# Performance work log

Hardware: AMD Instinct MI355X
Metric: run time of the kernel (lower is better)

Reference implementation:

```python
import jax, jax.numpy as jnp
import numpy as np

CPJ = 8
HID = 256
PARENTS = [-1,0,0,0,1,2,3,4,5,6,7,8,9,9,9,12,13,14,16,17,18,19]
SPARSE_IDX = list(range(54))

def _extend(nodes, cpj, parents=None):
    nodes = list(nodes)
    if parents is not None:
        while nodes[-1] != 0:
            nodes.append(parents[nodes[-1]])
    return [j * cpj + k for j in nodes for k in range(cpj)]

DQ_IN = _extend([0,3,6,9,12,13,14,15,16,17,18,19,20,21], CPJ, PARENTS)  # 21 nodes -> 168 ch
OUT1 = _extend([9], CPJ)          # 8 ch
OUT2 = _extend([6, 9, 12], CPJ)   # 24 ch
OUT3 = _extend([0, 3, 6], CPJ)    # 24 ch
IN_DIM = len(DQ_IN) + len(SPARSE_IDX)  # 222


def _mlp_params(key, out_dim):
    k = jax.random.split(key, 6)
    s = lambda fan_in: 1.0 / np.sqrt(fan_in)
    return (
        jax.random.uniform(k[0], (IN_DIM, HID), jnp.float32, -s(IN_DIM), s(IN_DIM)),
        jax.random.uniform(k[1], (HID,), jnp.float32, -s(IN_DIM), s(IN_DIM)),
        jax.random.uniform(k[2], (HID, HID), jnp.float32, -s(HID), s(HID)),
        jax.random.uniform(k[3], (HID,), jnp.float32, -s(HID), s(HID)),
        jax.random.uniform(k[4], (HID, out_dim), jnp.float32, -s(HID), s(HID)),
        jax.random.uniform(k[5], (out_dim,), jnp.float32, -s(HID), s(HID)),
    )


def setup_inputs() -> dict:
    key = jax.random.key(0)
    ks = jax.random.split(key, 5)
    B, T = 1024, 128
    inp = {
        'sparse_input': jax.random.normal(ks[0], (B, T, 54), jnp.float32),
        'decoder_output': jax.random.normal(ks[1], (B, T, 22 * CPJ), jnp.float32),
    }
    for i, (k, od) in enumerate(zip(ks[2:5], (len(OUT1), len(OUT2), len(OUT3))), start=1):
        p = _mlp_params(k, od)
        for j, name in enumerate(('w0', 'b0', 'w1', 'b1', 'w2', 'b2')):
            inp[f'{name}_{i}'] = p[j]
    return inp


def _mlp(x, w0, b0, w1, b1, w2, b2):
    h = jax.nn.leaky_relu(x @ w0 + b0, 0.01)
    h = jax.nn.leaky_relu(h @ w1 + b1, 0.01)
    return h @ w2 + b2


def reference(sparse_input, decoder_output,
              w0_1, b0_1, w1_1, b1_1, w2_1, b2_1,
              w0_2, b0_2, w1_2, b1_2, w2_2, b2_2,
              w0_3, b0_3, w1_3, b1_3, w2_3, b2_3):
    sp = sparse_input[:, :, jnp.array(SPARSE_IDX)]
    d = decoder_output
    # pass 1
    x = jnp.concatenate((d[:, :, jnp.array(DQ_IN)], sp), axis=2)
    res1 = _mlp(x, w0_1, b0_1, w1_1, b1_1, w2_1, b2_1)
    d = d.at[:, :, jnp.array(OUT1)].set(res1)
    # pass 2
    x = jnp.concatenate((d[:, :, jnp.array(DQ_IN)], sp), axis=2)
    res2 = _mlp(x, w0_2, b0_2, w1_2, b1_2, w2_2, b2_2)
    d = d.at[:, :, jnp.array(OUT2)].set(res2)
    # pass 3
    x = jnp.concatenate((d[:, :, jnp.array(DQ_IN)], sp), axis=2)
    res3 = _mlp(x, w0_3, b0_3, w1_3, b1_3, w2_3, b2_3)
    return res3
```

## Files before the change

### kernel.cpp

```cpp
#include <hip/hip_runtime.h>

typedef __bf16 bf16x8 __attribute__((ext_vector_type(8)));
typedef __bf16 bf16x4 __attribute__((ext_vector_type(4)));
typedef float  f32x16 __attribute__((ext_vector_type(16)));

#define DDEC  176
#define DSP   54
#define HID   256
#define RPW   32
#define WPB   8
#define BM    (RPW * WPB)
#define NTHR  (WPB * 64)
#define CSZ   8192
#define W1_OFF 65536
#define W2_OFF 131072
#define MLP_WS 139264

struct Biases { const float* b1[3]; const float* b2[3]; };

__global__ __launch_bounds__(256) void prep_weights(
    const float* __restrict__ w0a, const float* __restrict__ w1a, const float* __restrict__ w2a,
    const float* __restrict__ w0b, const float* __restrict__ w1b, const float* __restrict__ w2b,
    const float* __restrict__ w0c, const float* __restrict__ w1c, const float* __restrict__ w2c,
    const float* __restrict__ b0a, const float* __restrict__ b0b, const float* __restrict__ b0c,
    __bf16* __restrict__ ws)
{
  int idx = blockIdx.x * 256 + threadIdx.x;
  if (idx >= 3 * MLP_WS) return;
  int m = idx / MLP_WS;
  int r = idx - m * MLP_WS;
  const float* w0 = (m == 0) ? w0a : (m == 1) ? w0b : w0c;
  const float* w1 = (m == 0) ? w1a : (m == 1) ? w1b : w1c;
  const float* w2 = (m == 0) ? w2a : (m == 1) ? w2b : w2c;
  const float* b0 = (m == 0) ? b0a : (m == 1) ? b0b : b0c;
  float v;
  if (r < W1_OFF) {
    int n = r >> 8, k = r & 255;
    v = (k < 222) ? w0[k * HID + n] : (k == 222 ? b0[n] : 0.0f);
  } else if (r < W2_OFF) {
    int rr = r - W1_OFF;
    int n = rr >> 8, k = rr & 255;
    v = w1[k * HID + n];
  } else {
    int rr = r - W2_OFF;
    int n = rr >> 8, k = rr & 255;
    int od = (m == 0) ? 8 : 24;
    v = (n < od) ? w2[k * od + n] : 0.0f;
  }
  ws[idx] = (__bf16)v;
}

__device__ __forceinline__ float lrelu(float v) { return v > 0.f ? v : 0.01f * v; }

__device__ __forceinline__ void gload16(const void* g, void* l) {
  __builtin_amdgcn_global_load_lds(
      (const __attribute__((address_space(1))) void*)g,
      (__attribute__((address_space(3))) void*)l, 16, 0, 0);
}

__device__ __forceinline__ void stage(const __bf16* __restrict__ wsrc, __bf16* buf, int tid) {
  #pragma unroll
  for (int r = 0; r < 2; ++r) {
    const int a  = (r * NTHR + tid) * 16;
    const int lc = a >> 9;
    const int un = (a & 511) ^ ((lc & 31) << 4);
    gload16(wsrc + lc * 256 + (un >> 1), (char*)buf + r * (NTHR * 16) + (tid >> 6) * 1024);
  }
}

template<int NKK>
__device__ __forceinline__ void gemm1(const __bf16* buf, const bf16x8* bfr,
                                      f32x16& acc, int r32, int h) {
  const int sw = r32 << 4;
  const char* abase = (const char*)buf + (r32 << 9);
  #pragma unroll
  for (int kk = 0; kk < NKK; ++kk) {
    const int inner = ((kk << 5) + (h << 4)) ^ sw;
    bf16x8 a0 = *(const bf16x8*)(abase + inner);
    acc = __builtin_amdgcn_mfma_f32_32x32x16_bf16(a0, bfr[kk], acc, 0, 0, 0);
  }
}

__device__ __forceinline__ bf16x4 shfl32(bf16x4 x) {
  union { bf16x4 v; unsigned long long u; } t;
  t.v = x;
  t.u = __shfl_xor(t.u, 32, 64);
  return t.v;
}
__device__ __forceinline__ bf16x8 cat44(bf16x4 lo, bf16x4 hi) {
  return (bf16x8){lo[0], lo[1], lo[2], lo[3], hi[0], hi[1], hi[2], hi[3]};
}

struct Frag2 { bf16x8 f0, f1; };

template<bool BIAS, bool LR>
__device__ __forceinline__ Frag2 d2frags(const f32x16 acc, const float* bias, int h) {
  bf16x4 pk[4];
  #pragma unroll
  for (int t = 0; t < 4; ++t) {
    float bx = 0.f, by = 0.f, bz = 0.f, bw = 0.f;
    if (BIAS) {
      float4 bv = *(const float4*)(bias + 8 * t + 4 * h);
      bx = bv.x; by = bv.y; bz = bv.z; bw = bv.w;
    }
    float v0 = acc[4 * t] + bx, v1 = acc[4 * t + 1] + by;
    float v2 = acc[4 * t + 2] + bz, v3 = acc[4 * t + 3] + bw;
    if (LR) { v0 = lrelu(v0); v1 = lrelu(v1); v2 = lrelu(v2); v3 = lrelu(v3); }
    pk[t] = (bf16x4){(__bf16)v0, (__bf16)v1, (__bf16)v2, (__bf16)v3};
  }
  bf16x4 r1 = shfl32(h ? pk[0] : pk[1]);
  bf16x4 r2 = shfl32(h ? pk[2] : pk[3]);
  Frag2 out;
  out.f0 = h ? cat44(r1, pk[1]) : cat44(pk[0], r1);
  out.f1 = h ? cat44(r2, pk[3]) : cat44(pk[2], r2);
  return out;
}

__device__ __forceinline__ bf16x8 packf44(float4 a, float4 b) {
  return (bf16x8){(__bf16)a.x, (__bf16)a.y, (__bf16)a.z, (__bf16)a.w,
                  (__bf16)b.x, (__bf16)b.y, (__bf16)b.z, (__bf16)b.w};
}
__device__ __forceinline__ bf16x8 packf2222(float2 a, float2 b, float2 c, float2 d) {
  return (bf16x8){(__bf16)a.x, (__bf16)a.y, (__bf16)b.x, (__bf16)b.y,
                  (__bf16)c.x, (__bf16)c.y, (__bf16)d.x, (__bf16)d.y};
}

__global__ __launch_bounds__(NTHR, 2) void trunk_fused(
    const float* __restrict__ sparse, const float* __restrict__ dec,
    const __bf16* __restrict__ ws, float* __restrict__ out, Biases bp)
{
  __shared__ __align__(16) __bf16 lds[2 * CSZ];
  __bf16* const buf0 = lds;
  __bf16* const buf1 = lds + CSZ;

  const int tid  = threadIdx.x;
  const int lane = tid & 63;
  const int wid  = tid >> 6;
  const int r32  = lane & 31;
  const int h    = lane >> 5;
  const long grow = (long)blockIdx.x * BM + wid * RPW + r32;

  stage(ws, buf0, tid);

  bf16x8 xb[14];
  {
    constexpr int ND[21] = {0,3,6,9,12,13,14,15,16,17,18,19,20,21,19,17,14,9,6,3,0};
    const float* drow = dec + grow * DDEC;
    const float* srow = sparse + grow * DSP;
    #pragma unroll
    for (int kf = 0; kf < 14; ++kf) {
      if (kf <= 9) {
        const int off = (h ? ND[2 * kf + 1] : ND[2 * kf]) * 8;
        const float4* p = (const float4*)(drow + off);
        xb[kf] = packf44(p[0], p[1]);
      } else if (kf == 10) {
        if (h == 0) {
          const float4* p = (const float4*)(drow + ND[20] * 8);
          xb[kf] = packf44(p[0], p[1]);
        } else {
          const float2* q = (const float2*)(srow + 0);
          xb[kf] = packf2222(q[0], q[1], q[2], q[3]);
        }
      } else if (kf <= 12) {
        const float2* q = (const float2*)(srow + (2 * kf + h - 21) * 8);
        xb[kf] = packf2222(q[0], q[1], q[2], q[3]);
      } else {
        if (h == 0) {
          const float2* q = (const float2*)(srow + 40);
          xb[kf] = packf2222(q[0], q[1], q[2], q[3]);
        } else {
          const float2* q = (const float2*)(srow + 48);
          xb[kf] = packf2222(q[0], q[1], q[2], make_float2(1.0f, 0.0f));
        }
      }
    }
  }
  __syncthreads();
  int pb = 0;

  for (int m = 0; m < 3; ++m) {
    const __bf16* W0 = ws + m * MLP_WS;
    const __bf16* W1 = W0 + W1_OFF;
    const __bf16* W2 = W0 + W2_OFF;
    const float* b1 = bp.b1[m];
    const float* b2 = bp.b2[m];

    bf16x8 hb1[16];
    f32x16 a2 = {};

    #pragma unroll
    for (int c = 0; c < 8; ++c) {
      __bf16* cur = pb ? buf1 : buf0;
      __bf16* nxt = pb ? buf0 : buf1;
      stage(c < 7 ? W0 + (c + 1) * CSZ : W1, nxt, tid);
      f32x16 acc = {};
      gemm1<14>(cur, xb, acc, r32, h);
      Frag2 t = d2frags<false, true>(acc, nullptr, h);
      hb1[2 * c]     = t.f0;
      hb1[2 * c + 1] = t.f1;
      __syncthreads();
      pb ^= 1;
    }

    #pragma unroll
    for (int c = 0; c < 8; ++c) {
      __bf16* cur = pb ? buf1 : buf0;
      __bf16* nxt = pb ? buf0 : buf1;
      const __bf16* w2f = W2 + r32 * 256 + h * 8 + 32 * c;
      bf16x8 wa0 = *(const bf16x8*)(w2f + 0);
      bf16x8 wa1 = *(const bf16x8*)(w2f + 16);
      if (c < 7)      stage(W1 + (c + 1) * CSZ, nxt, tid);
      else if (m < 2) stage(ws + (m + 1) * MLP_WS, nxt, tid);
      f32x16 acc = {};
      gemm1<16>(cur, hb1, acc, r32, h);
      Frag2 t = d2frags<true, true>(acc, b1 + 32 * c, h);
      a2 = __builtin_amdgcn_mfma_f32_32x32x16_bf16(wa0, t.f0, a2, 0, 0, 0);
      a2 = __builtin_amdgcn_mfma_f32_32x32x16_bf16(wa1, t.f1, a2, 0, 0, 0);
      __syncthreads();
      pb ^= 1;
    }

    if (m == 2) {
      #pragma unroll
      for (int t = 0; t < 3; ++t) {
        const int c0 = 8 * t + 4 * h;
        float4 bv = *(const float4*)(b2 + c0);
        float4 o;
        o.x = a2[4 * t]     + bv.x;
        o.y = a2[4 * t + 1] + bv.y;
        o.z = a2[4 * t + 2] + bv.z;
        o.w = a2[4 * t + 3] + bv.w;
        *(float4*)(out + grow * 24 + c0) = o;
      }
    } else {
      bf16x4 pk[3];
      #pragma unroll
      for (int t = 0; t < 3; ++t) {
        const int c0 = 8 * t + 4 * h;
        float4 bv = *(const float4*)(b2 + c0);
        pk[t] = (bf16x4){(__bf16)(a2[4 * t] + bv.x),     (__bf16)(a2[4 * t + 1] + bv.y),
                         (__bf16)(a2[4 * t + 2] + bv.z), (__bf16)(a2[4 * t + 3] + bv.w)};
      }
      if (m == 0) {
        bf16x4 r = shfl32(pk[0]);
        if (h) { bf16x8 f = cat44(r, pk[0]); xb[1] = f; xb[8] = f; }
      } else {
        bf16x4 r1 = shfl32(h ? pk[0] : pk[1]);
        bf16x4 r2 = shfl32(pk[2]);
        if (h) {
          bf16x8 fJ9 = cat44(r1, pk[1]);  xb[1] = fJ9;  xb[8] = fJ9;
        } else {
          bf16x8 fJ6  = cat44(pk[0], r1); xb[1] = fJ6;  xb[9] = fJ6;
          bf16x8 fJ12 = cat44(pk[2], r2); xb[2] = fJ12;
        }
      }
    }
  }
}

extern "C" void kernel_launch(void* const* d_in, const int* in_sizes, int n_in,
                              void* d_out, int out_size, void* d_ws, size_t ws_size,
                              hipStream_t stream)
{
  const float* sparse = (const float*)d_in[0];
  const float* dec    = (const float*)d_in[1];
  Biases bp;
  const float* w0[3]; const float* w1[3]; const float* w2[3]; const float* b0[3];
  for (int m = 0; m < 3; ++m) {
    w0[m]    = (const float*)d_in[2 + m * 6 + 0];
    b0[m]    = (const float*)d_in[2 + m * 6 + 1];
    w1[m]    = (const float*)d_in[2 + m * 6 + 2];
    bp.b1[m] = (const float*)d_in[2 + m * 6 + 3];
    w2[m]    = (const float*)d_in[2 + m * 6 + 4];
    bp.b2[m] = (const float*)d_in[2 + m * 6 + 5];
  }
  __bf16* ws = (__bf16*)d_ws;
  const int nrows = in_sizes[0] / DSP;

  const int prep_total = 3 * MLP_WS;
  prep_weights<<<(prep_total + 255) / 256, 256, 0, stream>>>(
      w0[0], w1[0], w2[0], w0[1], w1[1], w2[1], w0[2], w1[2], w2[2],
      b0[0], b0[1], b0[2], ws);

  const int nblocks = nrows / BM;
  trunk_fused<<<nblocks, NTHR, 0, stream>>>(sparse, dec, ws, (float*)d_out, bp);
}
```

Baseline: 132.5 us.

## Deepen weight-staging pipeline to four LDS buffers with counted vmcnt waits

Replaces the double-buffered weight staging with a four-slot LDS ring that keeps three chunks in flight. A unified chunk index handles addressing across all three MLPs. Each iteration waits with an s_waitcnt vmcnt(4) plus barrier instead of a full __syncthreads, so outstanding prefetches are not drained. This aims to hide global-to-LDS latency, but it doubles LDS per block, which may hurt occupancy, and it relies on exact counting of outstanding memory ops for correctness.

```diff
diff --git a/kernel.cpp b/kernel.cpp
--- a/kernel.cpp
+++ b/kernel.cpp
@@ -68,6 +68,15 @@
   }
 }
 
+#define WAIT_BAR() asm volatile("s_waitcnt vmcnt(4)\n\ts_barrier" ::: "memory")
+
+__device__ __forceinline__ const __bf16* srcp(const __bf16* ws, int g) {
+  if (g > 47) g = 0;
+  const int m = g >> 4, c = g & 15;
+  const __bf16* base = ws + m * MLP_WS;
+  return (c < 8) ? (base + c * CSZ) : (base + W1_OFF + (c - 8) * CSZ);
+}
+
 template<int NKK>
 __device__ __forceinline__ void gemm1(const __bf16* buf, const bf16x8* bfr,
                                       f32x16& acc, int r32, int h) {
@@ -129,9 +138,7 @@
     const float* __restrict__ sparse, const float* __restrict__ dec,
     const __bf16* __restrict__ ws, float* __restrict__ out, Biases bp)
 {
-  __shared__ __align__(16) __bf16 lds[2 * CSZ];
-  __bf16* const buf0 = lds;
-  __bf16* const buf1 = lds + CSZ;
+  __shared__ __align__(16) __bf16 lds[4 * CSZ];
 
   const int tid  = threadIdx.x;
   const int lane = tid & 63;
@@ -140,7 +147,9 @@
   const int h    = lane >> 5;
   const long grow = (long)blockIdx.x * BM + wid * RPW + r32;
 
-  stage(ws, buf0, tid);
+  stage(srcp(ws, 0), lds + 0 * CSZ, tid);
+  stage(srcp(ws, 1), lds + 1 * CSZ, tid);
+  stage(srcp(ws, 2), lds + 2 * CSZ, tid);
 
   bf16x8 xb[14];
   {
@@ -176,12 +185,10 @@
     }
   }
   __syncthreads();
-  int pb = 0;
-
+
+  #pragma unroll
   for (int m = 0; m < 3; ++m) {
-    const __bf16* W0 = ws + m * MLP_WS;
-    const __bf16* W1 = W0 + W1_OFF;
-    const __bf16* W2 = W0 + W2_OFF;
+    const __bf16* W2 = ws + m * MLP_WS + W2_OFF;
     const float* b1 = bp.b1[m];
     const float* b2 = bp.b2[m];
 
@@ -190,34 +197,29 @@
 
     #pragma unroll
     for (int c = 0; c < 8; ++c) {
-      __bf16* cur = pb ? buf1 : buf0;
-      __bf16* nxt = pb ? buf0 : buf1;
-      stage(c < 7 ? W0 + (c + 1) * CSZ : W1, nxt, tid);
+      const int g = m * 16 + c;
+      WAIT_BAR();
+      stage(srcp(ws, g + 3), lds + ((g + 3) & 3) * CSZ, tid);
       f32x16 acc = {};
-      gemm1<14>(cur, xb, acc, r32, h);
+      gemm1<14>(lds + (g & 3) * CSZ, xb, acc, r32, h);
       Frag2 t = d2frags<false, true>(acc, nullptr, h);
       hb1[2 * c]     = t.f0;
       hb1[2 * c + 1] = t.f1;
-      __syncthreads();
-      pb ^= 1;
     }
 
     #pragma unroll
     for (int c = 0; c < 8; ++c) {
-      __bf16* cur = pb ? buf1 : buf0;
-      __bf16* nxt = pb ? buf0 : buf1;
+      const int g = m * 16 + 8 + c;
+      WAIT_BAR();
+      stage(srcp(ws, g + 3), lds + ((g + 3) & 3) * CSZ, tid);
       const __bf16* w2f = W2 + r32 * 256 + h * 8 + 32 * c;
       bf16x8 wa0 = *(const bf16x8*)(w2f + 0);
       bf16x8 wa1 = *(const bf16x8*)(w2f + 16);
-      if (c < 7)      stage(W1 + (c + 1) * CSZ, nxt, tid);
-      else if (m < 2) stage(ws + (m + 1) * MLP_WS, nxt, tid);
       f32x16 acc = {};
-      gemm1<16>(cur, hb1, acc, r32, h);
+      gemm1<16>(lds + (g & 3) * CSZ, hb1, acc, r32, h);
       Frag2 t = d2frags<true, true>(acc, b1 + 32 * c, h);
       a2 = __builtin_amdgcn_mfma_f32_32x32x16_bf16(wa0, t.f0, a2, 0, 0, 0);
       a2 = __builtin_amdgcn_mfma_f32_32x32x16_bf16(wa1, t.f1, a2, 0, 0, 0);
-      __syncthreads();
-      pb ^= 1;
     }
 
     if (m == 2) {
```

Measured after the change: 133.9 us. Within noise of the previous version (+1.1%).

## Pair LDS-staged and direct-global weight chunks per pipeline step

Applied to the files above, without the earlier changes.

Each pipeline step of the first two GEMMs now handles two weight chunks. One chunk comes from the LDS double buffer as before, and the other is read straight from global memory (L2) into registers, each feeding its own accumulator. This halves the number of LDS staging rounds and __syncthreads barriers per MLP and gives the MFMA chain two independent accumulators. The MLP loop is also fully unrolled. The trade-offs are exposed global-load latency inside the MFMA loop, higher VGPR pressure and larger code size.

```diff
diff --git a/kernel.cpp b/kernel.cpp
--- a/kernel.cpp
+++ b/kernel.cpp
@@ -69,15 +69,19 @@
 }
 
 template<int NKK>
-__device__ __forceinline__ void gemm1(const __bf16* buf, const bf16x8* bfr,
-                                      f32x16& acc, int r32, int h) {
+__device__ __forceinline__ void gemm_mix(const __bf16* lbuf, const __bf16* __restrict__ gsrc,
+                                         const bf16x8* bfr, f32x16& accL, f32x16& accG,
+                                         int r32, int h) {
   const int sw = r32 << 4;
-  const char* abase = (const char*)buf + (r32 << 9);
+  const char* abase = (const char*)lbuf + (r32 << 9);
+  const char* gbase = (const char*)gsrc + (r32 << 9);
   #pragma unroll
   for (int kk = 0; kk < NKK; ++kk) {
-    const int inner = ((kk << 5) + (h << 4)) ^ sw;
-    bf16x8 a0 = *(const bf16x8*)(abase + inner);
-    acc = __builtin_amdgcn_mfma_f32_32x32x16_bf16(a0, bfr[kk], acc, 0, 0, 0);
+    const int off = (kk << 5) + (h << 4);
+    bf16x8 aL = *(const bf16x8*)(abase + (off ^ sw));
+    bf16x8 aG = *(const bf16x8*)(gbase + off);
+    accL = __builtin_amdgcn_mfma_f32_32x32x16_bf16(aL, bfr[kk], accL, 0, 0, 0);
+    accG = __builtin_amdgcn_mfma_f32_32x32x16_bf16(aG, bfr[kk], accG, 0, 0, 0);
   }
 }
 
@@ -178,6 +182,7 @@
   __syncthreads();
   int pb = 0;
 
+  #pragma unroll
   for (int m = 0; m < 3; ++m) {
     const __bf16* W0 = ws + m * MLP_WS;
     const __bf16* W1 = W0 + W1_OFF;
@@ -189,33 +194,39 @@
     f32x16 a2 = {};
 
     #pragma unroll
-    for (int c = 0; c < 8; ++c) {
+    for (int p = 0; p < 4; ++p) {
       __bf16* cur = pb ? buf1 : buf0;
       __bf16* nxt = pb ? buf0 : buf1;
-      stage(c < 7 ? W0 + (c + 1) * CSZ : W1, nxt, tid);
-      f32x16 acc = {};
-      gemm1<14>(cur, xb, acc, r32, h);
-      Frag2 t = d2frags<false, true>(acc, nullptr, h);
-      hb1[2 * c]     = t.f0;
-      hb1[2 * c + 1] = t.f1;
+      stage(p < 3 ? W0 + (2 * p + 2) * CSZ : W1, nxt, tid);
+      f32x16 accL = {}, accG = {};
+      gemm_mix<14>(cur, W0 + (2 * p + 1) * CSZ, xb, accL, accG, r32, h);
+      Frag2 tL = d2frags<false, true>(accL, nullptr, h);
+      Frag2 tG = d2frags<false, true>(accG, nullptr, h);
+      hb1[4 * p]     = tL.f0;  hb1[4 * p + 1] = tL.f1;
+      hb1[4 * p + 2] = tG.f0;  hb1[4 * p + 3] = tG.f1;
       __syncthreads();
       pb ^= 1;
     }
 
     #pragma unroll
-    for (int c = 0; c < 8; ++c) {
+    for (int p = 0; p < 4; ++p) {
       __bf16* cur = pb ? buf1 : buf0;
       __bf16* nxt = pb ? buf0 : buf1;
-      const __bf16* w2f = W2 + r32 * 256 + h * 8 + 32 * c;
+      if (p < 3)      stage(W1 + (2 * p + 2) * CSZ, nxt, tid);
+      else if (m < 2) stage(ws + (m + 1) * MLP_WS, nxt, tid);
+      const __bf16* w2f = W2 + r32 * 256 + h * 8 + 64 * p;
       bf16x8 wa0 = *(const bf16x8*)(w2f + 0);
       bf16x8 wa1 = *(const bf16x8*)(w2f + 16);
-      if (c < 7)      stage(W1 + (c + 1) * CSZ, nxt, tid);
-      else if (m < 2) stage(ws + (m + 1) * MLP_WS, nxt, tid);
-      f32x16 acc = {};
-      gemm1<16>(cur, hb1, acc, r32, h);
-      Frag2 t = d2frags<true, true>(acc, b1 + 32 * c, h);
-      a2 = __builtin_amdgcn_mfma_f32_32x32x16_bf16(wa0, t.f0, a2, 0, 0, 0);
-      a2 = __builtin_amdgcn_mfma_f32_32x32x16_bf16(wa1, t.f1, a2, 0, 0, 0);
+      bf16x8 wa2 = *(const bf16x8*)(w2f + 32);
+      bf16x8 wa3 = *(const bf16x8*)(w2f + 48);
+      f32x16 accL = {}, accG = {};
+      gemm_mix<16>(cur, W1 + (2 * p + 1) * CSZ, hb1, accL, accG, r32, h);
+      Frag2 tL = d2frags<true, true>(accL, b1 + 64 * p, h);
+      Frag2 tG = d2frags<true, true>(accG, b1 + 64 * p + 32, h);
+      a2 = __builtin_amdgcn_mfma_f32_32x32x16_bf16(wa0, tL.f0, a2, 0, 0, 0);
+      a2 = __builtin_amdgcn_mfma_f32_32x32x16_bf16(wa1, tL.f1, a2, 0, 0, 0);
+      a2 = __builtin_amdgcn_mfma_f32_32x32x16_bf16(wa2, tG.f0, a2, 0, 0, 0);
+      a2 = __builtin_amdgcn_mfma_f32_32x32x16_bf16(wa3, tG.f1, a2, 0, 0, 0);
       __syncthreads();
       pb ^= 1;
     }
```

After: 265.4 us. 2x slower.

## Keep MLP weights in registers and stream 32-row activation tiles through LDS

Applied to the files above, without the earlier changes.

Each block now handles 512 rows, and each wave holds a 32-column slice of W0/W1/W2 in registers for one MLP pass. The block then loops over 16 tiles of 32 rows, with activations staged in LDS and double-buffered with prefetch of the next tile's inputs. This removes the per-block restreaming of all weight chunks through LDS. In exchange, the layer-3 output needs a cross-wave reduction through LDS, and the per-tile __syncthreads count rises. The whole block (16 tiles x 3 passes) is also serialized, the grid shrinks to 256 blocks, and register pressure is high.

```diff
diff --git a/kernel.cpp b/kernel.cpp
--- a/kernel.cpp
+++ b/kernel.cpp
@@ -2,19 +2,20 @@
 
 typedef __bf16 bf16x8 __attribute__((ext_vector_type(8)));
 typedef __bf16 bf16x4 __attribute__((ext_vector_type(4)));
+typedef float  f32x4v __attribute__((ext_vector_type(4)));
 typedef float  f32x16 __attribute__((ext_vector_type(16)));
 
 #define DDEC  176
 #define DSP   54
-#define HID   256
-#define RPW   32
-#define WPB   8
-#define BM    (RPW * WPB)
-#define NTHR  (WPB * 64)
-#define CSZ   8192
+#define RT    32
+#define NTILE 16
+#define BROWS (RT * NTILE)
+#define NTHR  512
 #define W1_OFF 65536
 #define W2_OFF 131072
 #define MLP_WS 139264
+
+__constant__ int c_nd[21] = {0,3,6,9,12,13,14,15,16,17,18,19,20,21,19,17,14,9,6,3,0};
 
 struct Biases { const float* b1[3]; const float* b2[3]; };
 
@@ -36,11 +37,11 @@
   float v;
   if (r < W1_OFF) {
     int n = r >> 8, k = r & 255;
-    v = (k < 222) ? w0[k * HID + n] : (k == 222 ? b0[n] : 0.0f);
+    v = (k < 222) ? w0[k * 256 + n] : (k == 222 ? b0[n] : 0.0f);
   } else if (r < W2_OFF) {
     int rr = r - W1_OFF;
     int n = rr >> 8, k = rr & 255;
-    v = w1[k * HID + n];
+    v = w1[k * 256 + n];
   } else {
     int rr = r - W2_OFF;
     int n = rr >> 8, k = rr & 255;
@@ -52,35 +53,6 @@
 
 __device__ __forceinline__ float lrelu(float v) { return v > 0.f ? v : 0.01f * v; }
 
-__device__ __forceinline__ void gload16(const void* g, void* l) {
-  __builtin_amdgcn_global_load_lds(
-      (const __attribute__((address_space(1))) void*)g,
-      (__attribute__((address_space(3))) void*)l, 16, 0, 0);
-}
-
-__device__ __forceinline__ void stage(const __bf16* __restrict__ wsrc, __bf16* buf, int tid) {
-  #pragma unroll
-  for (int r = 0; r < 2; ++r) {
-    const int a  = (r * NTHR + tid) * 16;
-    const int lc = a >> 9;
-    const int un = (a & 511) ^ ((lc & 31) << 4);
-    gload16(wsrc + lc * 256 + (un >> 1), (char*)buf + r * (NTHR * 16) + (tid >> 6) * 1024);
-  }
-}
-
-template<int NKK>
-__device__ __forceinline__ void gemm1(const __bf16* buf, const bf16x8* bfr,
-                                      f32x16& acc, int r32, int h) {
-  const int sw = r32 << 4;
-  const char* abase = (const char*)buf + (r32 << 9);
-  #pragma unroll
-  for (int kk = 0; kk < NKK; ++kk) {
-    const int inner = ((kk << 5) + (h << 4)) ^ sw;
-    bf16x8 a0 = *(const bf16x8*)(abase + inner);
-    acc = __builtin_amdgcn_mfma_f32_32x32x16_bf16(a0, bfr[kk], acc, 0, 0, 0);
-  }
-}
-
 __device__ __forceinline__ bf16x4 shfl32(bf16x4 x) {
   union { bf16x4 v; unsigned long long u; } t;
   t.v = x;
@@ -89,6 +61,10 @@
 }
 __device__ __forceinline__ bf16x8 cat44(bf16x4 lo, bf16x4 hi) {
   return (bf16x8){lo[0], lo[1], lo[2], lo[3], hi[0], hi[1], hi[2], hi[3]};
+}
+__device__ __forceinline__ bf16x8 packf44(float4 a, float4 b) {
+  return (bf16x8){(__bf16)a.x, (__bf16)a.y, (__bf16)a.z, (__bf16)a.w,
+                  (__bf16)b.x, (__bf16)b.y, (__bf16)b.z, (__bf16)b.w};
 }
 
 struct Frag2 { bf16x8 f0, f1; };
@@ -116,67 +92,70 @@
   return out;
 }
 
-__device__ __forceinline__ bf16x8 packf44(float4 a, float4 b) {
-  return (bf16x8){(__bf16)a.x, (__bf16)a.y, (__bf16)a.z, (__bf16)a.w,
-                  (__bf16)b.x, (__bf16)b.y, (__bf16)b.z, (__bf16)b.w};
-}
-__device__ __forceinline__ bf16x8 packf2222(float2 a, float2 b, float2 c, float2 d) {
-  return (bf16x8){(__bf16)a.x, (__bf16)a.y, (__bf16)b.x, (__bf16)b.y,
-                  (__bf16)c.x, (__bf16)c.y, (__bf16)d.x, (__bf16)d.y};
+struct GR { float4 a, b; };
+
+__device__ __forceinline__ GR load_gran(const float* __restrict__ drow,
+                                        const float* __restrict__ srow, int g, int nd) {
+  GR o;
+  if (g < 21) {
+    const float4* p = (const float4*)(drow + nd * 8);
+    o.a = p[0]; o.b = p[1];
+  } else if (g < 27) {
+    const float2* q = (const float2*)(srow + 8 * (g - 21));
+    o.a = make_float4(q[0].x, q[0].y, q[1].x, q[1].y);
+    o.b = make_float4(q[2].x, q[2].y, q[3].x, q[3].y);
+  } else if (g == 27) {
+    const float2* q = (const float2*)(srow + 48);
+    o.a = make_float4(q[0].x, q[0].y, q[1].x, q[1].y);
+    o.b = make_float4(q[2].x, q[2].y, 1.0f, 0.0f);
+  } else {
+    o.a = make_float4(0.f, 0.f, 0.f, 0.f); o.b = o.a;
+  }
+  return o;
+}
+
+__device__ __forceinline__ void write_gran(__bf16* xb, const __bf16* resrow,
+                                           int r, int g, int mp, GR v) {
+  int src = -1;
+  if (mp == 1)      { if (g == 3 || g == 17) src = 0; }
+  else if (mp == 2) { if (g == 2 || g == 18) src = 0;
+                      else if (g == 3 || g == 17) src = 8;
+                      else if (g == 4) src = 16; }
+  bf16x8 val = (src >= 0) ? *(const bf16x8*)(resrow + src) : packf44(v.a, v.b);
+  *(bf16x8*)(xb + r * 256 + ((g ^ r) & 31) * 8) = val;
 }
 
 __global__ __launch_bounds__(NTHR, 2) void trunk_fused(
     const float* __restrict__ sparse, const float* __restrict__ dec,
     const __bf16* __restrict__ ws, float* __restrict__ out, Biases bp)
 {
-  __shared__ __align__(16) __bf16 lds[2 * CSZ];
-  __bf16* const buf0 = lds;
-  __bf16* const buf1 = lds + CSZ;
+  __shared__ __align__(16) __bf16 xbuf[2 * 8192];
+  __shared__ __align__(16) __bf16 hbuf[8192];
+  __shared__ __align__(16) float  rbuf[8 * 1024];
+  __shared__ __align__(16) __bf16 resb[BROWS * 32];
 
   const int tid  = threadIdx.x;
   const int lane = tid & 63;
   const int wid  = tid >> 6;
   const int r32  = lane & 31;
   const int h    = lane >> 5;
-  const long grow = (long)blockIdx.x * BM + wid * RPW + r32;
-
-  stage(ws, buf0, tid);
-
-  bf16x8 xb[14];
+  const long row0 = (long)blockIdx.x * BROWS;
+
+  const int gr = tid >> 4;
+  const int g0 = (tid & 15) * 2;
+  const int g1 = g0 + 1;
+  const int nd0 = (g0 < 21) ? c_nd[g0] : 0;
+  const int nd1 = (g1 < 21) ? c_nd[g1] : 0;
+
   {
-    constexpr int ND[21] = {0,3,6,9,12,13,14,15,16,17,18,19,20,21,19,17,14,9,6,3,0};
-    const float* drow = dec + grow * DDEC;
-    const float* srow = sparse + grow * DSP;
-    #pragma unroll
-    for (int kf = 0; kf < 14; ++kf) {
-      if (kf <= 9) {
-        const int off = (h ? ND[2 * kf + 1] : ND[2 * kf]) * 8;
-        const float4* p = (const float4*)(drow + off);
-        xb[kf] = packf44(p[0], p[1]);
-      } else if (kf == 10) {
-        if (h == 0) {
-          const float4* p = (const float4*)(drow + ND[20] * 8);
-          xb[kf] = packf44(p[0], p[1]);
-        } else {
-          const float2* q = (const float2*)(srow + 0);
-          xb[kf] = packf2222(q[0], q[1], q[2], q[3]);
-        }
-      } else if (kf <= 12) {
-        const float2* q = (const float2*)(srow + (2 * kf + h - 21) * 8);
-        xb[kf] = packf2222(q[0], q[1], q[2], q[3]);
-      } else {
-        if (h == 0) {
-          const float2* q = (const float2*)(srow + 40);
-          xb[kf] = packf2222(q[0], q[1], q[2], q[3]);
-        } else {
-          const float2* q = (const float2*)(srow + 48);
-          xb[kf] = packf2222(q[0], q[1], q[2], make_float2(1.0f, 0.0f));
-        }
-      }
-    }
+    const float* drow = dec + (row0 + gr) * DDEC;
+    const float* srow = sparse + (row0 + gr) * DSP;
+    GR v0 = load_gran(drow, srow, g0, nd0);
+    GR v1 = load_gran(drow, srow, g1, nd1);
+    write_gran(xbuf, resb, gr, g0, 0, v0);
+    write_gran(xbuf, resb, gr, g1, 0, v1);
   }
   __syncthreads();
-  int pb = 0;
 
   for (int m = 0; m < 3; ++m) {
     const __bf16* W0 = ws + m * MLP_WS;
@@ -185,75 +164,95 @@
     const float* b1 = bp.b1[m];
     const float* b2 = bp.b2[m];
 
-    bf16x8 hb1[16];
-    f32x16 a2 = {};
-
-    #pragma unroll
-    for (int c = 0; c < 8; ++c) {
-      __bf16* cur = pb ? buf1 : buf0;
-      __bf16* nxt = pb ? buf0 : buf1;
-      stage(c < 7 ? W0 + (c + 1) * CSZ : W1, nxt, tid);
+    bf16x8 w0r[14], w1r[16], w2r[2];
+    {
+      const __bf16* p0 = W0 + (size_t)(32 * wid + r32) * 256 + 8 * h;
+      #pragma unroll
+      for (int kk = 0; kk < 14; ++kk) w0r[kk] = *(const bf16x8*)(p0 + 16 * kk);
+      const __bf16* p1 = W1 + (size_t)(32 * wid + r32) * 256 + 8 * h;
+      #pragma unroll
+      for (int kk = 0; kk < 16; ++kk) w1r[kk] = *(const bf16x8*)(p1 + 16 * kk);
+      const __bf16* p2 = W2 + (size_t)r32 * 256 + 32 * wid + 8 * h;
+      w2r[0] = *(const bf16x8*)(p2);
+      w2r[1] = *(const bf16x8*)(p2 + 16);
+    }
+
+    for (int t = 0; t < NTILE; ++t) {
+      const int p = t & 1;
+      const __bf16* xcur = xbuf + p * 8192;
+
       f32x16 acc = {};
-      gemm1<14>(cur, xb, acc, r32, h);
-      Frag2 t = d2frags<false, true>(acc, nullptr, h);
-      hb1[2 * c]     = t.f0;
-      hb1[2 * c + 1] = t.f1;
+      {
+        const __bf16* xrow = xcur + r32 * 256;
+        #pragma unroll
+        for (int kk = 0; kk < 14; ++kk) {
+          bf16x8 bfr = *(const bf16x8*)(xrow + (((2 * kk + h) ^ r32) & 31) * 8);
+          acc = __builtin_amdgcn_mfma_f32_32x32x16_bf16(w0r[kk], bfr, acc, 0, 0, 0);
+        }
+      }
+      Frag2 th1 = d2frags<false, true>(acc, nullptr, h);
+      {
+        __bf16* hrow = hbuf + r32 * 256;
+        *(bf16x8*)(hrow + (((4 * wid + h) ^ r32) & 31) * 8)     = th1.f0;
+        *(bf16x8*)(hrow + (((4 * wid + 2 + h) ^ r32) & 31) * 8) = th1.f1;
+      }
       __syncthreads();
-      pb ^= 1;
-    }
-
-    #pragma unroll
-    for (int c = 0; c < 8; ++c) {
-      __bf16* cur = pb ? buf1 : buf0;
-      __bf16* nxt = pb ? buf0 : buf1;
-      const __bf16* w2f = W2 + r32 * 256 + h * 8 + 32 * c;
-      bf16x8 wa0 = *(const bf16x8*)(w2f + 0);
-      bf16x8 wa1 = *(const bf16x8*)(w2f + 16);
-      if (c < 7)      stage(W1 + (c + 1) * CSZ, nxt, tid);
-      else if (m < 2) stage(ws + (m + 1) * MLP_WS, nxt, tid);
-      f32x16 acc = {};
-      gemm1<16>(cur, hb1, acc, r32, h);
-      Frag2 t = d2frags<true, true>(acc, b1 + 32 * c, h);
-      a2 = __builtin_amdgcn_mfma_f32_32x32x16_bf16(wa0, t.f0, a2, 0, 0, 0);
-      a2 = __builtin_amdgcn_mfma_f32_32x32x16_bf16(wa1, t.f1, a2, 0, 0, 0);
+
+      const int gphase = m * NTILE + t;
+      const bool dopf = (gphase + 1 < 3 * NTILE);
+      GR v0, v1;
+      if (dopf) {
+        const long nrow = row0 + ((t + 1 < NTILE) ? (t + 1) * RT : 0) + gr;
+        const float* drow = dec + nrow * DDEC;
+        const float* srow = sparse + nrow * DSP;
+        v0 = load_gran(drow, srow, g0, nd0);
+        v1 = load_gran(drow, srow, g1, nd1);
+      }
+
+      f32x16 acc1 = {};
+      {
+        const __bf16* hrow = hbuf + r32 * 256;
+        #pragma unroll
+        for (int kk = 0; kk < 16; ++kk) {
+          bf16x8 bfr = *(const bf16x8*)(hrow + (((2 * kk + h) ^ r32) & 31) * 8);
+          acc1 = __builtin_amdgcn_mfma_f32_32x32x16_bf16(w1r[kk], bfr, acc1, 0, 0, 0);
+        }
+      }
+      Frag2 th2 = d2frags<true, true>(acc1, b1 + 32 * wid, h);
+
+      f32x16 a2 = {};
+      a2 = __builtin_amdgcn_mfma_f32_32x32x16_bf16(w2r[0], th2.f0, a2, 0, 0, 0);
+      a2 = __builtin_amdgcn_mfma_f32_32x32x16_bf16(w2r[1], th2.f1, a2, 0, 0, 0);
+      {
+        float* rb = rbuf + wid * 1024 + r32 * 32;
+        #pragma unroll
+        for (int q = 0; q < 4; ++q) {
+          f32x4v val = {a2[4 * q], a2[4 * q + 1], a2[4 * q + 2], a2[4 * q + 3]};
+          *(f32x4v*)(rb + 4 * (((2 * q + h) ^ (r32 & 7)) & 7)) = val;
+        }
+      }
       __syncthreads();
-      pb ^= 1;
-    }
-
-    if (m == 2) {
-      #pragma unroll
-      for (int t = 0; t < 3; ++t) {
-        const int c0 = 8 * t + 4 * h;
-        float4 bv = *(const float4*)(b2 + c0);
-        float4 o;
-        o.x = a2[4 * t]     + bv.x;
-        o.y = a2[4 * t + 1] + bv.y;
-        o.z = a2[4 * t + 2] + bv.z;
-        o.w = a2[4 * t + 3] + bv.w;
-        *(float4*)(out + grow * 24 + c0) = o;
-      }
-    } else {
-      bf16x4 pk[3];
-      #pragma unroll
-      for (int t = 0; t < 3; ++t) {
-        const int c0 = 8 * t + 4 * h;
-        float4 bv = *(const float4*)(b2 + c0);
-        pk[t] = (bf16x4){(__bf16)(a2[4 * t] + bv.x),     (__bf16)(a2[4 * t + 1] + bv.y),
-                         (__bf16)(a2[4 * t + 2] + bv.z), (__bf16)(a2[4 * t + 3] + bv.w)};
-      }
-      if (m == 0) {
-        bf16x4 r = shfl32(pk[0]);
-        if (h) { bf16x8 f = cat44(r, pk[0]); xb[1] = f; xb[8] = f; }
-      } else {
-        bf16x4 r1 = shfl32(h ? pk[0] : pk[1]);
-        bf16x4 r2 = shfl32(pk[2]);
-        if (h) {
-          bf16x8 fJ9 = cat44(r1, pk[1]);  xb[1] = fJ9;  xb[8] = fJ9;
-        } else {
-          bf16x8 fJ6  = cat44(pk[0], r1); xb[1] = fJ6;  xb[9] = fJ6;
-          bf16x8 fJ12 = cat44(pk[2], r2); xb[2] = fJ12;
-        }
-      }
+
+      for (int i = tid; i < 768; i += NTHR) {
+        const int c = i % 24;
+        const int r = i / 24;
+        const int ro = r * 32 + 4 * (((c >> 2) ^ (r & 7)) & 7) + (c & 3);
+        float s = 0.f;
+        #pragma unroll
+        for (int w = 0; w < 8; ++w) s += rbuf[w * 1024 + ro];
+        s += b2[c];
+        if (m == 2) out[(row0 + t * RT + r) * 24 + c] = s;
+        else        resb[(t * RT + r) * 32 + c] = (__bf16)s;
+      }
+      if (dopf) {
+        const int mp = (t + 1 < NTILE) ? m : m + 1;
+        const int tn = (t + 1 < NTILE) ? t + 1 : 0;
+        __bf16* xnxt = xbuf + (p ^ 1) * 8192;
+        const __bf16* resrow = resb + (tn * RT + gr) * 32;
+        write_gran(xnxt, resrow, gr, g0, mp, v0);
+        write_gran(xnxt, resrow, gr, g1, mp, v1);
+      }
+      __syncthreads();
     }
   }
 }
@@ -282,6 +281,6 @@
       w0[0], w1[0], w2[0], w0[1], w1[1], w2[1], w0[2], w1[2], w2[2],
       b0[0], b0[1], b0[2], ws);
 
-  const int nblocks = nrows / BM;
+  const int nblocks = nrows / BROWS;
   trunk_fused<<<nblocks, NTHR, 0, stream>>>(sparse, dec, ws, (float*)d_out, bp);
 }
```

Measured after the change: 188.1 us. 42.0% more time.
